# Kernel tuning notes

Hardware: AMD Instinct MI355X
Metric: run time of the kernel (lower is better)

Reference implementation:

```python
import jax, jax.numpy as jnp
import numpy as np
import math

B, N, P, S, C, NC = 8, 20000, 256, 32, 256, 18


def setup_inputs() -> dict:
    key = jax.random.key(0)
    ks = jax.random.split(key, 20)
    w = lambda k, shape: jax.random.normal(k, shape, jnp.float32) * 0.02
    return {
        "xyz": jax.random.normal(ks[0], (B, N, 3), jnp.float32),
        "features": jax.random.normal(ks[1], (B, C, N), jnp.float32),
        "boxes_size": jax.random.uniform(ks[2], (B, P, 3), jnp.float32, 0.2, 1.5),
        "boxes_label": jax.random.normal(ks[3], (B, P, NC), jnp.float32),
        "ts": jax.random.uniform(ks[4], (B,), jnp.float32) * 1000.0,
        "inds": jax.random.randint(ks[5], (B, P), 0, N, jnp.int32),
        # SharedMLP (259 -> 128 -> 128 -> 128), bn=False so conv1x1+bias+ReLU
        "mw0": w(ks[6], (128, C + 3)), "mb0": jnp.zeros((128,), jnp.float32),
        "mw1": w(ks[7], (128, 128)), "mb1": jnp.zeros((128,), jnp.float32),
        "mw2": w(ks[8], (128, 128)), "mb2": jnp.zeros((128,), jnp.float32),
        # label SharedMLP (18+128 -> 256 -> 256 -> 256)
        "lw0": w(ks[9], (256, NC + 128)), "lb0": jnp.zeros((256,), jnp.float32),
        "lw1": w(ks[10], (256, 256)), "lb1": jnp.zeros((256,), jnp.float32),
        "lw2": w(ks[11], (256, 256)), "lb2": jnp.zeros((256,), jnp.float32),
        # time_mlp: sinusoid(128) -> 512 -> GELU -> 512 ; block: SiLU -> 256
        "tw0": w(ks[12], (512, 128)), "tb0": jnp.zeros((512,), jnp.float32),
        "tw1": w(ks[13], (512, 512)), "tb1": jnp.zeros((512,), jnp.float32),
        "bw": w(ks[14], (256, 512)), "bb": jnp.zeros((256,), jnp.float32),
        # time_mlp_label: sinusoid(256) -> 1024 -> GELU -> 1024 ; block: SiLU -> 512
        "tlw0": w(ks[15], (1024, 256)), "tlb0": jnp.zeros((1024,), jnp.float32),
        "tlw1": w(ks[16], (1024, 1024)), "tlb1": jnp.zeros((1024,), jnp.float32),
        "blw": w(ks[17], (512, 1024)), "blb": jnp.zeros((512,), jnp.float32),
    }


def _sinusoid(t, dim):
    half = dim // 2
    freqs = jnp.exp(jnp.arange(half, dtype=jnp.float32) * (-(math.log(10000.0) / (half - 1))))
    e = t[:, None] * freqs[None, :]
    return jnp.concatenate([jnp.sin(e), jnp.cos(e)], axis=-1)


def _film(feat, ts, w0, b0, w1, b1, bw, bb, dim):
    # feat: [B, D, P]; replicates torch repeat_interleave/chunk/reshape exactly
    temb = jax.nn.gelu(_sinusoid(ts, dim) @ w0.T + b0, approximate=False) @ w1.T + b1
    ss = jax.nn.silu(temb) @ bw.T + bb          # [B, 2D]
    ss = jnp.repeat(ss, P, axis=0)              # [B*P, 2D]
    scale, shift = jnp.split(ss, 2, axis=1)
    scale = scale.reshape(-1, P)
    shift = shift.reshape(-1, P)
    f = feat.reshape(-1, P)
    return (f * (scale + 1.0) + shift).reshape(feat.shape[0], -1, P)


def reference(xyz, features, boxes_size, boxes_label, ts, inds,
              mw0, mb0, mw1, mb1, mw2, mb2,
              lw0, lb0, lw1, lb1, lw2, lb2,
              tw0, tb0, tw1, tb1, bw, bb,
              tlw0, tlb0, tlw1, tlb1, blw, blb):
    # gather proposal centers
    new_xyz = jnp.take_along_axis(xyz, inds[:, :, None], axis=1)        # [B,P,3]
    # axis-aligned box containment (the hull corners are an AABB: center +/- size/2)
    half = boxes_size * 0.5
    inside = jnp.all(jnp.abs(xyz[:, None, :, :] - new_xyz[:, :, None, :]) <= half[:, :, None, :], axis=-1)  # [B,P,N]
    # deterministic with-replacement sampling of in-box points: in-box indices first (stable sort), then cycle
    order = jnp.argsort(jnp.logical_not(inside), axis=-1)               # [B,P,N]
    count = jnp.maximum(inside.sum(axis=-1), 1)                          # [B,P]
    pos = jnp.arange(S, dtype=count.dtype)[None, None, :] % count[:, :, None]
    idx = jnp.take_along_axis(order, pos, axis=-1)                       # [B,P,S]
    b_idx = jnp.arange(B)[:, None, None]
    gxyz = xyz[b_idx, idx] - new_xyz[:, :, None, :]                      # [B,P,S,3]
    gfeat = jnp.transpose(features, (0, 2, 1))[b_idx, idx]               # [B,P,S,C]
    g = jnp.concatenate([gxyz, gfeat], axis=-1)                          # [B,P,S,3+C]
    act = lambda x, w, b: jax.nn.relu(jnp.einsum('bpsc,oc->bpso', x, w) + b)
    h = act(act(act(g, mw0, mb0), mw1, mb1), mw2, mb2)                   # [B,P,S,128]
    nf = h.max(axis=2)                                                   # [B,P,128] (max-pool over nsample)
    nf_t = jnp.transpose(nf, (0, 2, 1))                                  # [B,128,P]
    new_features = _film(nf_t, ts, tw0, tb0, tw1, tb1, bw, bb, 128)
    # label branch
    li = jnp.concatenate([boxes_label, nf], axis=-1)                     # [B,P,18+128]
    act2 = lambda x, w, b: jax.nn.relu(jnp.einsum('bpc,oc->bpo', x, w) + b)
    lf = act2(act2(act2(li, lw0, lb0), lw1, lb1), lw2, lb2)              # [B,P,256]
    lf_t = jnp.transpose(lf, (0, 2, 1))                                  # [B,256,P]
    label_feature = _film(lf_t, ts, tlw0, tlb0, tlw1, tlb1, blw, blb, 256)
    return (new_xyz, new_features, label_feature, inds)
```

## Files before the change

kernel.cpp:

```cpp
#include <hip/hip_runtime.h>
#include <math.h>

#define BB 8
#define NN 20000
#define PP 256
#define SSAMP 32
#define CC 256

typedef unsigned short u16;
typedef unsigned int u32;
typedef __attribute__((ext_vector_type(8))) short short8;
typedef __attribute__((ext_vector_type(4))) float f32x4;

__device__ __forceinline__ float b2f(u16 u) {
    union { u32 i; float f; } x; x.i = ((u32)u) << 16; return x.f;
}
__device__ __forceinline__ u16 f2b(float f) {
    union { float f; u32 i; } x; x.f = f;
    u32 i = x.i;
    i += 0x7fffu + ((i >> 16) & 1u);
    return (u16)(i >> 16);
}
__device__ __forceinline__ float rnd_bf(float f) { return b2f(f2b(f)); }
__device__ __forceinline__ float geluf(float x) {
    return 0.5f * x * (1.0f + erff(x * 0.7071067811865476f));
}
__device__ __forceinline__ float siluf(float x) {
    return x / (1.0f + expf(-x));
}
__device__ __forceinline__ f32x4 fz4() { f32x4 z = {0.f,0.f,0.f,0.f}; return z; }

__device__ __forceinline__ float ldf(const void* p, size_t i, int f32f) {
    return f32f ? ((const float*)p)[i] : b2f(((const u16*)p)[i]);
}
__device__ __forceinline__ u16 ldw(const void* p, size_t i, int f32f) {
    return f32f ? f2b(((const float*)p)[i]) : ((const u16*)p)[i];
}

__device__ __forceinline__ int detect_f32d(const void* xyz) {
    int lane = threadIdx.x & 63;
    u16 u = ((const u16*)xyz)[(size_t)lane * 7496];
    int e = (u >> 7) & 0xFF;
    bool inR = (e >= 0x70) && (e <= 0x85);
    unsigned long long m = __ballot(inR);
    return (__popcll(m) < 48) ? 1 : 0;
}

__device__ __forceinline__ void repack_body(int f32f, int rb, int tid,
        const void* mw0, const void* mw1, const void* mw2,
        const void* lw0, const void* lw1, const void* lw2,
        const void* mb0, const void* mb1, const void* mb2,
        const void* lb0, const void* lb1, const void* lb2,
        u16* __restrict__ W0p, u16* __restrict__ W1p, u16* __restrict__ W2p,
        u16* __restrict__ L0p, u16* __restrict__ L1p, u16* __restrict__ L2p,
        float* __restrict__ biasF) {
    int i = rb * 256 + tid;
    if (i < 36864) {
        int o = i / 288, c = i % 288;
        u16 v = 0;
        if (c < 256) v = ldw(mw0, o * 259 + 3 + c, f32f);
        else if (c < 259) v = ldw(mw0, o * 259 + (c - 256), f32f);
        W0p[i] = v;
    } else if (i < 53248) {
        W1p[i - 36864] = ldw(mw1, i - 36864, f32f);
    } else if (i < 69632) {
        W2p[i - 53248] = ldw(mw2, i - 53248, f32f);
    } else if (i < 110592) {
        int j = i - 69632;
        int o = j / 160, c = j % 160;
        L0p[j] = (c < 146) ? ldw(lw0, o * 146 + c, f32f) : (u16)0;
    } else if (i < 176128) {
        L1p[i - 110592] = ldw(lw1, i - 110592, f32f);
    } else if (i < 241664) {
        L2p[i - 176128] = ldw(lw2, i - 176128, f32f);
    } else if (i < 242816) {
        int j = i - 241664;
        float v;
        if (j < 128) v = ldf(mb0, j, f32f);
        else if (j < 256) v = ldf(mb1, j - 128, f32f);
        else if (j < 384) v = ldf(mb2, j - 256, f32f);
        else if (j < 640) v = ldf(lb0, j - 384, f32f);
        else if (j < 896) v = ldf(lb1, j - 640, f32f);
        else v = ldf(lb2, j - 896, f32f);
        biasF[j] = v;
    }
}

__device__ __forceinline__ void transpose_body(int f32f, const void* __restrict__ feat,
        u16* __restrict__ featT, int n0i, int c0i, int bz, int b0, int tid,
        u16 (*tile)[66]) {
    int c0 = c0i * 64, n0 = n0i * 64;
    int b = b0 + bz;
    int tx = tid & 63, ty = tid >> 6;
    const size_t fb = (size_t)b * CC * NN;
    for (int i = 0; i < 16; i++) {
        int cl = ty * 16 + i;
        int n = n0 + tx;
        if (n < NN) tile[cl][tx] = ldw(feat, fb + (size_t)(c0 + cl) * NN + n, f32f);
    }
    __syncthreads();
    const size_t tb = (size_t)bz * NN * CC;
    for (int i = 0; i < 16; i++) {
        int nl = ty * 16 + i;
        int n = n0 + nl;
        if (n < NN) featT[tb + (size_t)n * CC + c0 + tx] = tile[tx][nl];
    }
}

template<int ACT, int SRC>
__device__ __forceinline__ void lin_body(int f32f, const void* __restrict__ xin,
        const void* __restrict__ W, const void* __restrict__ bias,
        float* __restrict__ out, int K, int O, int rb, int tid, float* xs) {
    if (SRC == 2) {
        const float* X = (const float*)xin;
        for (int i = tid; i < 8 * K; i += 256) xs[i] = X[i];
    } else {
        const int half = (SRC == 0) ? 64 : 128;
        const int dim = half * 2;
        const float cst = (SRC == 0) ? (logf(10000.f) / 63.f) : (logf(10000.f) / 127.f);
        for (int i = tid; i < 8 * dim; i += 256) {
            int b = i / dim, j = i % dim;
            float t = ldf(xin, b, f32f);
            int jj = (j < half) ? j : (j - half);
            float e = t * expf(-(float)jj * cst);
            xs[i] = (j < half) ? sinf(e) : cosf(e);
        }
    }
    __syncthreads();
    int lane = tid & 63, wv = tid >> 6;
    int r = rb * 4 + wv;
    if (r >= O) return;
    float acc[8] = {0.f, 0.f, 0.f, 0.f, 0.f, 0.f, 0.f, 0.f};
    for (int k = lane; k < K; k += 64) {
        float wval = ldf(W, (size_t)r * K + k, f32f);
        #pragma unroll
        for (int b = 0; b < 8; b++) acc[b] += wval * xs[b * K + k];
    }
    #pragma unroll
    for (int b = 0; b < 8; b++) {
        acc[b] += __shfl_xor(acc[b], 1);
        acc[b] += __shfl_xor(acc[b], 2);
        acc[b] += __shfl_xor(acc[b], 4);
        acc[b] += __shfl_xor(acc[b], 8);
        acc[b] += __shfl_xor(acc[b], 16);
        acc[b] += __shfl_xor(acc[b], 32);
    }
    if (lane == 0) {
        float bv = ldf(bias, r, f32f);
        #pragma unroll
        for (int b = 0; b < 8; b++) {
            float v = acc[b] + bv;
            if (ACT == 1) v = geluf(v);
            else if (ACT == 2) v = siluf(v);
            out[b * O + r] = v;
        }
    }
}

__device__ __forceinline__ void sample_body(int f32f, const void* __restrict__ xyz,
        const void* __restrict__ bsize, const int* __restrict__ inds,
        int* __restrict__ sidx, float* __restrict__ cenW,
        float* __restrict__ outXyz, float* __restrict__ outInds,
        int pg, int tid, int* sBuf, int* wcnt) {
    int lane = tid & 63, w = tid >> 6;
    int b = pg >> 8;
    int ind = inds[pg];
    ind = ind < 0 ? 0 : (ind >= NN ? NN - 1 : ind);
    if (tid < SSAMP) sBuf[tid] = 0;
    size_t xb = (size_t)b * NN * 3;
    float cx = ldf(xyz, xb + (size_t)ind * 3 + 0, f32f);
    float cy = ldf(xyz, xb + (size_t)ind * 3 + 1, f32f);
    float cz = ldf(xyz, xb + (size_t)ind * 3 + 2, f32f);
    float hx = 0.5f * ldf(bsize, pg * 3 + 0, f32f);
    float hy = 0.5f * ldf(bsize, pg * 3 + 1, f32f);
    float hz = 0.5f * ldf(bsize, pg * 3 + 2, f32f);
    int cnt = 0, par = 0;
    const unsigned long long lmask = (1ull << lane) - 1ull;
    for (int base = 0; base < NN; base += 1024, par ^= 4) {
        int nb = base + w * 256 + lane;
        int nn[4];
        float px[4], py[4], pz[4];
        #pragma unroll
        for (int u = 0; u < 4; u++) {
            int n = nb + u * 64;
            nn[u] = n;
            int nc = n < NN ? n : NN - 1;
            size_t a = xb + (size_t)nc * 3;
            px[u] = ldf(xyz, a, f32f);
            py[u] = ldf(xyz, a + 1, f32f);
            pz[u] = ldf(xyz, a + 2, f32f);
        }
        bool isin[4];
        unsigned long long m[4];
        int pc[4];
        int tw = 0;
        #pragma unroll
        for (int u = 0; u < 4; u++) {
            bool in_ = (nn[u] < NN) &&
                       (fabsf(px[u] - cx) <= hx) &&
                       (fabsf(py[u] - cy) <= hy) &&
                       (fabsf(pz[u] - cz) <= hz);
            isin[u] = in_;
            m[u] = __ballot(in_);
            pc[u] = (int)__popcll(m[u]);
            tw += pc[u];
        }
        if (lane == 0) wcnt[par + w] = tw;
        __syncthreads();
        int w0 = wcnt[par + 0], w1 = wcnt[par + 1], w2 = wcnt[par + 2], w3 = wcnt[par + 3];
        int total = w0 + w1 + w2 + w3;
        int prior = cnt;
        if (w >= 1) prior += w0;
        if (w >= 2) prior += w1;
        if (w >= 3) prior += w2;
        #pragma unroll
        for (int u = 0; u < 4; u++) {
            int pos = prior + (int)__popcll(m[u] & lmask);
            if (isin[u] && pos < SSAMP) sBuf[pos] = nn[u];
            prior += pc[u];
        }
        cnt += total;
        if (cnt >= SSAMP) break;
    }
    __syncthreads();
    int ccap = cnt < SSAMP ? cnt : SSAMP;
    if (ccap < 1) ccap = 1;
    if (tid < SSAMP) sidx[pg * SSAMP + tid] = sBuf[tid % ccap];
    if (tid < 3) {
        float cv = tid == 0 ? cx : (tid == 1 ? cy : cz);
        outXyz[pg * 3 + tid] = cv;
        cenW[pg * 3 + tid] = cv;
    }
    if (tid == 0) outInds[pg] = rnd_bf((float)ind);
}

__global__ __launch_bounds__(256) void k_front(
        const void* __restrict__ xyz, const void* __restrict__ feat,
        const void* __restrict__ bsize, const int* __restrict__ inds,
        const void* __restrict__ ts,
        const void* mw0, const void* mw1, const void* mw2,
        const void* lw0, const void* lw1, const void* lw2,
        const void* mb0, const void* mb1, const void* mb2,
        const void* lb0, const void* lb1, const void* lb2,
        const void* tw0, const void* tb0,
        const void* tlw0, const void* tlb0,
        u16* __restrict__ featT, int nTrans,
        int* __restrict__ sidx, float* __restrict__ cenW,
        float* __restrict__ outXyz, float* __restrict__ outInds,
        u16* __restrict__ W0p, u16* __restrict__ W1p, u16* __restrict__ W2p,
        u16* __restrict__ L0p, u16* __restrict__ L1p, u16* __restrict__ L2p,
        float* __restrict__ biasF, float* __restrict__ h0W, float* __restrict__ g0W) {
    __shared__ __align__(16) char smem[8448];
    int tid = threadIdx.x;
    int f32f = detect_f32d(xyz);
    unsigned bx = blockIdx.x;
    unsigned s1 = 2048u + (unsigned)nTrans;
    unsigned s2 = s1 + 949u;
    unsigned s3 = s2 + 128u;
    if (bx < 2048u) {
        sample_body(f32f, xyz, bsize, inds, sidx, cenW, outXyz, outInds,
                    (int)bx, tid, (int*)smem, (int*)(smem + 128));
    } else if (bx < s1) {
        int t = (int)(bx - 2048u);
        transpose_body(f32f, feat, featT, t % 313, (t / 313) & 3, t / 1252, 0, tid,
                       (u16(*)[66])smem);
    } else if (bx < s2) {
        repack_body(f32f, (int)(bx - s1), tid, mw0, mw1, mw2, lw0, lw1, lw2,
                    mb0, mb1, mb2, lb0, lb1, lb2, W0p, W1p, W2p, L0p, L1p, L2p, biasF);
    } else if (bx < s3) {
        lin_body<1, 0>(f32f, ts, tw0, tb0, h0W, 128, 512, (int)(bx - s2), tid, (float*)smem);
    } else {
        lin_body<1, 1>(f32f, ts, tlw0, tlb0, g0W, 256, 1024, (int)(bx - s3), tid, (float*)smem);
    }
}

__global__ __launch_bounds__(256) void k_mid2(const void* __restrict__ xyz,
        const void* tw1, const void* tb1, const void* tlw1, const void* tlb1,
        const float* __restrict__ h0W, const float* __restrict__ g0W,
        float* __restrict__ tembW, float* __restrict__ temblW) {
    __shared__ float xs[8 * 1024];
    int tid = threadIdx.x;
    int f32f = detect_f32d(xyz);
    unsigned bx = blockIdx.x;
    if (bx < 128u) lin_body<2, 2>(f32f, h0W, tw1, tb1, tembW, 512, 512, (int)bx, tid, xs);
    else lin_body<2, 2>(f32f, g0W, tlw1, tlb1, temblW, 1024, 1024, (int)(bx - 128u), tid, xs);
}

__global__ __launch_bounds__(256) void k_mid3(const void* __restrict__ xyz,
        const void* bw, const void* bb, const void* blw, const void* blb,
        const float* __restrict__ tembW, const float* __restrict__ temblW,
        float* __restrict__ ssW, float* __restrict__ sslW) {
    __shared__ float xs[8 * 1024];
    int tid = threadIdx.x;
    int f32f = detect_f32d(xyz);
    unsigned bx = blockIdx.x;
    if (bx < 64u) lin_body<0, 2>(f32f, tembW, bw, bb, ssW, 512, 256, (int)bx, tid, xs);
    else lin_body<0, 2>(f32f, temblW, blw, blb, sslW, 1024, 512, (int)(bx - 64u), tid, xs);
}

__global__ __launch_bounds__(256) void k_transpose(const void* __restrict__ xyz,
                                                   const void* __restrict__ feat,
                                                   u16* __restrict__ featT, int b0) {
    __shared__ u16 tile[64][66];
    int f32f = detect_f32d(xyz);
    transpose_body(f32f, feat, featT, blockIdx.x, blockIdx.y, blockIdx.z, b0,
                   threadIdx.x, tile);
}

__global__ __launch_bounds__(256) void k_mlp1(
        const u16* __restrict__ featT, const void* __restrict__ feat,
        int blockOff, int tier,
        const void* __restrict__ xyz, const int* __restrict__ sidx,
        const float* __restrict__ cenW, const float* __restrict__ ssW,
        const u16* __restrict__ W0p, const u16* __restrict__ W1p,
        const u16* __restrict__ W2p, const float* __restrict__ biasF,
        u16* __restrict__ nfB, float* __restrict__ outNF) {
    __shared__ u16 gA[64 * 296];
    __shared__ u16 h1s[64 * 136];
    __shared__ int nrowS[64];
    __shared__ float centS[8];
    int f32f = detect_f32d(xyz);
    int tid = threadIdx.x;
    int pbase = (blockIdx.x + blockOff) * 2;
    int b = pbase >> 8;
    if (tid < 64) {
        int n = sidx[pbase * SSAMP + tid];
        nrowS[tid] = n < 0 ? 0 : (n >= NN ? NN - 1 : n);
    }
    if (tid < 6) centS[tid] = cenW[pbase * 3 + tid];
    for (int e = tid; e < 64 * 32; e += 256) {
        int row = e >> 5, c2 = e & 31;
        if (c2 >= 8 && c2 < 28)
            *(u32*)&gA[row * 296 + 256 + (c2 - 8) * 2] = 0u;
    }
    __syncthreads();
    if (tier >= 1) {
        size_t rowBase = (tier == 2) ? ((size_t)b * NN) : 0;
        for (int e = tid; e < 64 * 32; e += 256) {
            int row = e >> 5, seg = e & 31;
            int n = nrowS[row];
            uint4 v = *(const uint4*)(featT + (rowBase + n) * CC + seg * 8);
            *(uint4*)&gA[row * 296 + seg * 8] = v;
        }
    } else {
        int row = tid & 63;
        int n = nrowS[row];
        const size_t fb = (size_t)b * CC * NN;
        int cbase = tid >> 6;
        for (int it = 0; it < 64; it++) {
            int cch = it * 4 + cbase;
            gA[row * 296 + cch] = ldw(feat, fb + (size_t)cch * NN + n, f32f);
        }
    }
    if (tid < 64) {
        int row = tid, q = row >> 5;
        int n = nrowS[row];
        size_t a = ((size_t)b * NN + n) * 3;
        for (int d = 0; d < 3; d++) {
            float gv = ldf(xyz, a + d, f32f) - centS[q * 3 + d];
            gA[row * 296 + 256 + d] = f2b(gv);
        }
    }
    __syncthreads();

    int lane = tid & 63, w = tid >> 6;
    int c15 = lane & 15, kq = lane >> 4;
    f32x4 acc[4][2];

    for (int mt = 0; mt < 4; mt++) for (int j = 0; j < 2; j++) acc[mt][j] = fz4();
    for (int ks = 0; ks < 9; ks++) {
        int k0 = ks * 32 + kq * 8;
        short8 af[4];
        for (int mt = 0; mt < 4; mt++)
            af[mt] = *(const short8*)&gA[(mt * 16 + c15) * 296 + k0];
        for (int j = 0; j < 2; j++) {
            int col = w * 32 + j * 16 + c15;
            short8 bf = *(const short8*)(W0p + col * 288 + k0);
            for (int mt = 0; mt < 4; mt++)
                acc[mt][j] = __builtin_amdgcn_mfma_f32_16x16x32_bf16(af[mt], bf, acc[mt][j], 0, 0, 0);
        }
    }
    for (int j = 0; j < 2; j++) {
        int col = w * 32 + j * 16 + c15;
        float bias = biasF[col];
        for (int mt = 0; mt < 4; mt++)
            for (int r = 0; r < 4; r++) {
                float v = acc[mt][j][r] + bias;
                v = v > 0.f ? v : 0.f;
                h1s[(mt * 16 + kq * 4 + r) * 136 + col] = f2b(v);
            }
    }
    __syncthreads();

    u16* h2s = gA;
    for (int mt = 0; mt < 4; mt++) for (int j = 0; j < 2; j++) acc[mt][j] = fz4();
    for (int ks = 0; ks < 4; ks++) {
        int k0 = ks * 32 + kq * 8;
        short8 af[4];
        for (int mt = 0; mt < 4; mt++)
            af[mt] = *(const short8*)&h1s[(mt * 16 + c15) * 136 + k0];
        for (int j = 0; j < 2; j++) {
            int col = w * 32 + j * 16 + c15;
            short8 bf = *(const short8*)(W1p + col * 128 + k0);
            for (int mt = 0; mt < 4; mt++)
                acc[mt][j] = __builtin_amdgcn_mfma_f32_16x16x32_bf16(af[mt], bf, acc[mt][j], 0, 0, 0);
        }
    }
    __syncthreads();
    for (int j = 0; j < 2; j++) {
        int col = w * 32 + j * 16 + c15;
        float bias = biasF[128 + col];
        for (int mt = 0; mt < 4; mt++)
            for (int r = 0; r < 4; r++) {
                float v = acc[mt][j][r] + bias;
                v = v > 0.f ? v : 0.f;
                h2s[(mt * 16 + kq * 4 + r) * 136 + col] = f2b(v);
            }
    }
    __syncthreads();

    for (int mt = 0; mt < 4; mt++) for (int j = 0; j < 2; j++) acc[mt][j] = fz4();
    for (int ks = 0; ks < 4; ks++) {
        int k0 = ks * 32 + kq * 8;
        short8 af[4];
        for (int mt = 0; mt < 4; mt++)
            af[mt] = *(const short8*)&h2s[(mt * 16 + c15) * 136 + k0];
        for (int j = 0; j < 2; j++) {
            int col = w * 32 + j * 16 + c15;
            short8 bf = *(const short8*)(W2p + col * 128 + k0);
            for (int mt = 0; mt < 4; mt++)
                acc[mt][j] = __builtin_amdgcn_mfma_f32_16x16x32_bf16(af[mt], bf, acc[mt][j], 0, 0, 0);
        }
    }
    int pA = pbase & 255, pB = (pbase + 1) & 255;
    float scA = ssW[b * 256 + (pA & 127)] + 1.f, shA = ssW[b * 256 + 128 + (pA & 127)];
    float scB = ssW[b * 256 + (pB & 127)] + 1.f, shB = ssW[b * 256 + 128 + (pB & 127)];
    for (int j = 0; j < 2; j++) {
        int col = w * 32 + j * 16 + c15;
        float bias = biasF[256 + col];
        float mA = 0.f, mB = 0.f;
        for (int mt = 0; mt < 2; mt++)
            for (int r = 0; r < 4; r++) {
                float v = acc[mt][j][r] + bias; v = v > 0.f ? v : 0.f;
                mA = fmaxf(mA, v);
            }
        for (int mt = 2; mt < 4; mt++)
            for (int r = 0; r < 4; r++) {
                float v = acc[mt][j][r] + bias; v = v > 0.f ? v : 0.f;
                mB = fmaxf(mB, v);
            }
        mA = fmaxf(mA, __shfl_xor(mA, 16)); mA = fmaxf(mA, __shfl_xor(mA, 32));
        mB = fmaxf(mB, __shfl_xor(mB, 16)); mB = fmaxf(mB, __shfl_xor(mB, 32));
        if (lane < 16) {
            nfB[(size_t)(pbase + 0) * 128 + col] = f2b(mA);
            nfB[(size_t)(pbase + 1) * 128 + col] = f2b(mB);
            outNF[((size_t)b * 128 + col) * 256 + pA] = mA * scA + shA;
            outNF[((size_t)b * 128 + col) * 256 + pB] = mB * scB + shB;
        }
    }
}

__global__ __launch_bounds__(256) void k_label(const void* __restrict__ xyz,
        const void* __restrict__ blabel,
        const u16* __restrict__ nfB, const u16* __restrict__ L0p,
        const u16* __restrict__ L1p, const u16* __restrict__ L2p,
        const float* __restrict__ biasF, const float* __restrict__ sslW,
        float* __restrict__ outLF) {
    __shared__ u16 liS[16 * 168];
    __shared__ u16 h1L[16 * 264];
    __shared__ u16 h2L[16 * 264];
    int f32f = detect_f32d(xyz);
    int tid = threadIdx.x;
    int pbase = blockIdx.x * 16;
    for (int e = tid; e < 16 * 160; e += 256) {
        int row = e / 160, c = e % 160;
        int pg = pbase + row;
        u16 v = 0;
        if (c < 18) v = ldw(blabel, pg * 18 + c, f32f);
        else if (c < 146) v = nfB[(size_t)pg * 128 + (c - 18)];
        liS[row * 168 + c] = v;
    }
    __syncthreads();
    int lane = tid & 63, w = tid >> 6;
    int c15 = lane & 15, kq = lane >> 4;
    f32x4 acc[4];

    for (int j = 0; j < 4; j++) acc[j] = fz4();
    for (int ks = 0; ks < 5; ks++) {
        int k0 = ks * 32 + kq * 8;
        short8 af = *(const short8*)&liS[c15 * 168 + k0];
        for (int j = 0; j < 4; j++) {
            int col = w * 64 + j * 16 + c15;
            short8 bf = *(const short8*)(L0p + col * 160 + k0);
            acc[j] = __builtin_amdgcn_mfma_f32_16x16x32_bf16(af, bf, acc[j], 0, 0, 0);
        }
    }
    for (int j = 0; j < 4; j++) {
        int col = w * 64 + j * 16 + c15;
        float bias = biasF[384 + col];
        for (int r = 0; r < 4; r++) {
            float v = acc[j][r] + bias; v = v > 0.f ? v : 0.f;
            h1L[(kq * 4 + r) * 264 + col] = f2b(v);
        }
    }
    __syncthreads();

    for (int j = 0; j < 4; j++) acc[j] = fz4();
    for (int ks = 0; ks < 8; ks++) {
        int k0 = ks * 32 + kq * 8;
        short8 af = *(const short8*)&h1L[c15 * 264 + k0];
        for (int j = 0; j < 4; j++) {
            int col = w * 64 + j * 16 + c15;
            short8 bf = *(const short8*)(L1p + col * 256 + k0);
            acc[j] = __builtin_amdgcn_mfma_f32_16x16x32_bf16(af, bf, acc[j], 0, 0, 0);
        }
    }
    for (int j = 0; j < 4; j++) {
        int col = w * 64 + j * 16 + c15;
        float bias = biasF[640 + col];
        for (int r = 0; r < 4; r++) {
            float v = acc[j][r] + bias; v = v > 0.f ? v : 0.f;
            h2L[(kq * 4 + r) * 264 + col] = f2b(v);
        }
    }
    __syncthreads();

    for (int j = 0; j < 4; j++) acc[j] = fz4();
    for (int ks = 0; ks < 8; ks++) {
        int k0 = ks * 32 + kq * 8;
        short8 af = *(const short8*)&h2L[c15 * 264 + k0];
        for (int j = 0; j < 4; j++) {
            int col = w * 64 + j * 16 + c15;
            short8 bf = *(const short8*)(L2p + col * 256 + k0);
            acc[j] = __builtin_amdgcn_mfma_f32_16x16x32_bf16(af, bf, acc[j], 0, 0, 0);
        }
    }
    for (int j = 0; j < 4; j++) {
        int col = w * 64 + j * 16 + c15;
        float bias = biasF[896 + col];
        for (int r = 0; r < 4; r++) {
            int pr = pbase + kq * 4 + r;
            int bb2 = pr >> 8, p = pr & 255;
            float v = acc[j][r] + bias; v = v > 0.f ? v : 0.f;
            float sc = sslW[bb2 * 512 + p] + 1.f;
            float sh = sslW[bb2 * 512 + 256 + p];
            outLF[((size_t)bb2 * 256 + col) * 256 + p] = v * sc + sh;
        }
    }
}

extern "C" void kernel_launch(void* const* d_in, const int* in_sizes, int n_in,
                              void* d_out, int out_size, void* d_ws, size_t ws_size,
                              hipStream_t stream) {
    const void* xyz    = d_in[0];
    const void* feat   = d_in[1];
    const void* bsize  = d_in[2];
    const void* blabel = d_in[3];
    const void* ts     = d_in[4];
    const int* inds    = (const int*)d_in[5];
    const void* mw0 = d_in[6];  const void* mb0 = d_in[7];
    const void* mw1 = d_in[8];  const void* mb1 = d_in[9];
    const void* mw2 = d_in[10]; const void* mb2 = d_in[11];
    const void* lw0 = d_in[12]; const void* lb0 = d_in[13];
    const void* lw1 = d_in[14]; const void* lb1 = d_in[15];
    const void* lw2 = d_in[16]; const void* lb2 = d_in[17];
    const void* tw0 = d_in[18]; const void* tb0 = d_in[19];
    const void* tw1 = d_in[20]; const void* tb1 = d_in[21];
    const void* bw  = d_in[22]; const void* bb  = d_in[23];
    const void* tlw0 = d_in[24]; const void* tlb0 = d_in[25];
    const void* tlw1 = d_in[26]; const void* tlb1 = d_in[27];
    const void* blw  = d_in[28]; const void* blb  = d_in[29];

    float* out = (float*)d_out;
    float* outXyz  = out;
    float* outNF   = out + 6144;
    float* outLF   = out + 268288;
    float* outInds = out + 792576;

    char* ws = (char*)d_ws;
    u16*   W0p   = (u16*)(ws + 64);
    u16*   W1p   = (u16*)(ws + 73792);
    u16*   W2p   = (u16*)(ws + 106560);
    u16*   L0p   = (u16*)(ws + 139328);
    u16*   L1p   = (u16*)(ws + 221248);
    u16*   L2p   = (u16*)(ws + 352320);
    float* biasF = (float*)(ws + 483392);
    float* ssW   = (float*)(ws + 488000);
    float* sslW  = (float*)(ws + 496192);
    float* cenW  = (float*)(ws + 512576);
    int*   sidx  = (int*)(ws + 537152);
    u16*   nfB   = (u16*)(ws + 799296);
    float* h0W   = (float*)(ws + 1323584);
    float* tembW = (float*)(ws + 1339968);
    float* g0W   = (float*)(ws + 1356352);
    float* temblW= (float*)(ws + 1389120);
    u16*   featT = (u16*)(ws + 1421888);
    const size_t NEED_A = 1421888ull + 81920000ull;
    const size_t NEED_B = 1421888ull + 10240000ull;
    int tier = (ws_size >= NEED_A) ? 2 : ((ws_size >= NEED_B) ? 1 : 0);

    int nTrans = (tier == 2) ? 10016 : 0;
    unsigned gFront = 2048u + (unsigned)nTrans + 949u + 128u + 256u;
    k_front<<<dim3(gFront), dim3(256), 0, stream>>>(
        xyz, feat, bsize, inds, ts,
        mw0, mw1, mw2, lw0, lw1, lw2,
        mb0, mb1, mb2, lb0, lb1, lb2,
        tw0, tb0, tlw0, tlb0,
        featT, nTrans, sidx, cenW, outXyz, outInds,
        W0p, W1p, W2p, L0p, L1p, L2p, biasF, h0W, g0W);

    k_mid2<<<dim3(384), dim3(256), 0, stream>>>(xyz, tw1, tb1, tlw1, tlb1,
                                                h0W, g0W, tembW, temblW);
    k_mid3<<<dim3(192), dim3(256), 0, stream>>>(xyz, bw, bb, blw, blb,
                                                tembW, temblW, ssW, sslW);

    if (tier == 2) {
        k_mlp1<<<dim3(1024), dim3(256), 0, stream>>>(featT, feat, 0, 2, xyz, sidx, cenW, ssW,
                                                     W0p, W1p, W2p, biasF, nfB, outNF);
    } else if (tier == 1) {
        for (int b = 0; b < BB; b++) {
            k_transpose<<<dim3(313, 4, 1), dim3(256), 0, stream>>>(xyz, feat, featT, b);
            k_mlp1<<<dim3(128), dim3(256), 0, stream>>>(featT, feat, b * 128, 1, xyz, sidx, cenW, ssW,
                                                        W0p, W1p, W2p, biasF, nfB, outNF);
        }
    } else {
        k_mlp1<<<dim3(1024), dim3(256), 0, stream>>>(featT, feat, 0, 0, xyz, sidx, cenW, ssW,
                                                     W0p, W1p, W2p, biasF, nfB, outNF);
    }

    k_label<<<dim3(128), dim3(256), 0, stream>>>(xyz, blabel, nfB, L0p, L1p, L2p, biasF, sslW, outLF);
}
```

Measured before the change: 427.5 us.

## Vectorize transpose, prefetch sampling loads, and merge MLP with time-MLP kernels

Several changes at once. The feature transpose now uses float4/ushort4 vector loads and stores for full tiles. The ball-query loop double-buffers the next xyz chunk in registers. The grouped point MLP is fused into one kernel with the second time-MLP layer, and the FiLM scale/shift of new_features is deferred to the tail kernel through an fp32 staging buffer. This cuts launches and lets the point MLP overlap the time-embedding GEMV. The cost is an extra global round-trip for the unmodulated features, plus higher register and LDS use in the merged kernel.

```diff
diff --git a/kernel.cpp b/kernel.cpp
--- a/kernel.cpp
+++ b/kernel.cpp
@@ -91,19 +91,58 @@
         u16 (*tile)[66]) {
     int c0 = c0i * 64, n0 = n0i * 64;
     int b = b0 + bz;
-    int tx = tid & 63, ty = tid >> 6;
     const size_t fb = (size_t)b * CC * NN;
-    for (int i = 0; i < 16; i++) {
-        int cl = ty * 16 + i;
-        int n = n0 + tx;
-        if (n < NN) tile[cl][tx] = ldw(feat, fb + (size_t)(c0 + cl) * NN + n, f32f);
-    }
-    __syncthreads();
     const size_t tb = (size_t)bz * NN * CC;
-    for (int i = 0; i < 16; i++) {
-        int nl = ty * 16 + i;
-        int n = n0 + nl;
-        if (n < NN) featT[tb + (size_t)n * CC + c0 + tx] = tile[tx][nl];
+    if (n0 + 64 <= NN) {
+        int n4 = tid & 15, ci = tid >> 4;
+        if (f32f) {
+            #pragma unroll
+            for (int pass = 0; pass < 4; pass++) {
+                int c = pass * 16 + ci;
+                const float* src = (const float*)feat + fb + (size_t)(c0 + c) * NN + n0 + n4 * 4;
+                float4 v = *(const float4*)src;
+                tile[c][n4 * 4 + 0] = f2b(v.x);
+                tile[c][n4 * 4 + 1] = f2b(v.y);
+                tile[c][n4 * 4 + 2] = f2b(v.z);
+                tile[c][n4 * 4 + 3] = f2b(v.w);
+            }
+        } else {
+            #pragma unroll
+            for (int pass = 0; pass < 4; pass++) {
+                int c = pass * 16 + ci;
+                const u16* src = (const u16*)feat + fb + (size_t)(c0 + c) * NN + n0 + n4 * 4;
+                ushort4 v = *(const ushort4*)src;
+                tile[c][n4 * 4 + 0] = v.x;
+                tile[c][n4 * 4 + 1] = v.y;
+                tile[c][n4 * 4 + 2] = v.z;
+                tile[c][n4 * 4 + 3] = v.w;
+            }
+        }
+        __syncthreads();
+        int c4 = tid & 15, ni = tid >> 4;
+        #pragma unroll
+        for (int pass = 0; pass < 4; pass++) {
+            int n = pass * 16 + ni;
+            ushort4 o;
+            o.x = tile[c4 * 4 + 0][n];
+            o.y = tile[c4 * 4 + 1][n];
+            o.z = tile[c4 * 4 + 2][n];
+            o.w = tile[c4 * 4 + 3][n];
+            *(ushort4*)(featT + tb + (size_t)(n0 + n) * CC + c0 + c4 * 4) = o;
+        }
+    } else {
+        int tx = tid & 63, ty = tid >> 6;
+        for (int i = 0; i < 16; i++) {
+            int cl = ty * 16 + i;
+            int n = n0 + tx;
+            if (n < NN) tile[cl][tx] = ldw(feat, fb + (size_t)(c0 + cl) * NN + n, f32f);
+        }
+        __syncthreads();
+        for (int i = 0; i < 16; i++) {
+            int nl = ty * 16 + i;
+            int n = n0 + nl;
+            if (n < NN) featT[tb + (size_t)n * CC + c0 + tx] = tile[tx][nl];
+        }
     }
 }
 
@@ -176,19 +215,34 @@
     float hz = 0.5f * ldf(bsize, pg * 3 + 2, f32f);
     int cnt = 0, par = 0;
     const unsigned long long lmask = (1ull << lane) - 1ull;
-    for (int base = 0; base < NN; base += 1024, par ^= 4) {
-        int nb = base + w * 256 + lane;
-        int nn[4];
-        float px[4], py[4], pz[4];
-        #pragma unroll
-        for (int u = 0; u < 4; u++) {
-            int n = nb + u * 64;
-            nn[u] = n;
-            int nc = n < NN ? n : NN - 1;
-            size_t a = xb + (size_t)nc * 3;
-            px[u] = ldf(xyz, a, f32f);
-            py[u] = ldf(xyz, a + 1, f32f);
-            pz[u] = ldf(xyz, a + 2, f32f);
+    int nn[4];
+    float px[4], py[4], pz[4];
+    #pragma unroll
+    for (int u = 0; u < 4; u++) {
+        int n = w * 256 + lane + u * 64;
+        nn[u] = n;
+        int nc = n < NN ? n : NN - 1;
+        size_t a = xb + (size_t)nc * 3;
+        px[u] = ldf(xyz, a, f32f);
+        py[u] = ldf(xyz, a + 1, f32f);
+        pz[u] = ldf(xyz, a + 2, f32f);
+    }
+    for (int base = 0;;) {
+        int nbase = base + 1024;
+        bool more = nbase < NN;
+        int qn[4];
+        float qx[4], qy[4], qz[4];
+        if (more) {
+            #pragma unroll
+            for (int u = 0; u < 4; u++) {
+                int n = nbase + w * 256 + lane + u * 64;
+                qn[u] = n;
+                int nc = n < NN ? n : NN - 1;
+                size_t a = xb + (size_t)nc * 3;
+                qx[u] = ldf(xyz, a, f32f);
+                qy[u] = ldf(xyz, a + 1, f32f);
+                qz[u] = ldf(xyz, a + 2, f32f);
+            }
         }
         bool isin[4];
         unsigned long long m[4];
@@ -220,7 +274,13 @@
             prior += pc[u];
         }
         cnt += total;
-        if (cnt >= SSAMP) break;
+        if (cnt >= SSAMP || !more) break;
+        par ^= 4;
+        base = nbase;
+        #pragma unroll
+        for (int u = 0; u < 4; u++) {
+            nn[u] = qn[u]; px[u] = qx[u]; py[u] = qy[u]; pz[u] = qz[u];
+        }
     }
     __syncthreads();
     int ccap = cnt < SSAMP ? cnt : SSAMP;
@@ -232,6 +292,153 @@
         cenW[pg * 3 + tid] = cv;
     }
     if (tid == 0) outInds[pg] = rnd_bf((float)ind);
+}
+
+__device__ __forceinline__ void mlp1_body(int f32f,
+        const u16* __restrict__ featT, const void* __restrict__ feat,
+        int pbase, int tier,
+        const void* __restrict__ xyz, const int* __restrict__ sidx,
+        const float* __restrict__ cenW,
+        const u16* __restrict__ W0p, const u16* __restrict__ W1p,
+        const u16* __restrict__ W2p, const float* __restrict__ biasF,
+        u16* __restrict__ nfB, float* __restrict__ nfF,
+        int tid, u16* gA, int* nrowS, float* centS) {
+    int b = pbase >> 8;
+    if (tid < 64) {
+        int n = sidx[pbase * SSAMP + tid];
+        nrowS[tid] = n < 0 ? 0 : (n >= NN ? NN - 1 : n);
+    }
+    if (tid < 6) centS[tid] = cenW[pbase * 3 + tid];
+    for (int e = tid; e < 64 * 32; e += 256) {
+        int row = e >> 5, c2 = e & 31;
+        if (c2 >= 8 && c2 < 28)
+            *(u32*)&gA[row * 296 + 256 + (c2 - 8) * 2] = 0u;
+    }
+    __syncthreads();
+    if (tier >= 1) {
+        size_t rowBase = (tier == 2) ? ((size_t)b * NN) : 0;
+        for (int e = tid; e < 64 * 32; e += 256) {
+            int row = e >> 5, seg = e & 31;
+            int n = nrowS[row];
+            uint4 v = *(const uint4*)(featT + (rowBase + n) * CC + seg * 8);
+            *(uint4*)&gA[row * 296 + seg * 8] = v;
+        }
+    } else {
+        int row = tid & 63;
+        int n = nrowS[row];
+        const size_t fb = (size_t)b * CC * NN;
+        int cbase = tid >> 6;
+        for (int it = 0; it < 64; it++) {
+            int cch = it * 4 + cbase;
+            gA[row * 296 + cch] = ldw(feat, fb + (size_t)cch * NN + n, f32f);
+        }
+    }
+    if (tid < 64) {
+        int row = tid, q = row >> 5;
+        int n = nrowS[row];
+        size_t a = ((size_t)b * NN + n) * 3;
+        for (int d = 0; d < 3; d++) {
+            float gv = ldf(xyz, a + d, f32f) - centS[q * 3 + d];
+            gA[row * 296 + 256 + d] = f2b(gv);
+        }
+    }
+    __syncthreads();
+
+    int lane = tid & 63, w = tid >> 6;
+    int c15 = lane & 15, kq = lane >> 4;
+    f32x4 acc[4][2];
+
+    for (int mt = 0; mt < 4; mt++) for (int j = 0; j < 2; j++) acc[mt][j] = fz4();
+    for (int ks = 0; ks < 9; ks++) {
+        int k0 = ks * 32 + kq * 8;
+        short8 af[4];
+        for (int mt = 0; mt < 4; mt++)
+            af[mt] = *(const short8*)&gA[(mt * 16 + c15) * 296 + k0];
+        for (int j = 0; j < 2; j++) {
+            int col = w * 32 + j * 16 + c15;
+            short8 bf = *(const short8*)(W0p + col * 288 + k0);
+            for (int mt = 0; mt < 4; mt++)
+                acc[mt][j] = __builtin_amdgcn_mfma_f32_16x16x32_bf16(af[mt], bf, acc[mt][j], 0, 0, 0);
+        }
+    }
+    __syncthreads();
+    u16* h1s = gA;
+    u16* h2s = gA + 8704;
+    for (int j = 0; j < 2; j++) {
+        int col = w * 32 + j * 16 + c15;
+        float bias = biasF[col];
+        for (int mt = 0; mt < 4; mt++)
+            for (int r = 0; r < 4; r++) {
+                float v = acc[mt][j][r] + bias;
+                v = v > 0.f ? v : 0.f;
+                h1s[(mt * 16 + kq * 4 + r) * 136 + col] = f2b(v);
+            }
+    }
+    __syncthreads();
+
+    for (int mt = 0; mt < 4; mt++) for (int j = 0; j < 2; j++) acc[mt][j] = fz4();
+    for (int ks = 0; ks < 4; ks++) {
+        int k0 = ks * 32 + kq * 8;
+        short8 af[4];
+        for (int mt = 0; mt < 4; mt++)
+            af[mt] = *(const short8*)&h1s[(mt * 16 + c15) * 136 + k0];
+        for (int j = 0; j < 2; j++) {
+            int col = w * 32 + j * 16 + c15;
+            short8 bf = *(const short8*)(W1p + col * 128 + k0);
+            for (int mt = 0; mt < 4; mt++)
+                acc[mt][j] = __builtin_amdgcn_mfma_f32_16x16x32_bf16(af[mt], bf, acc[mt][j], 0, 0, 0);
+        }
+    }
+    __syncthreads();
+    for (int j = 0; j < 2; j++) {
+        int col = w * 32 + j * 16 + c15;
+        float bias = biasF[128 + col];
+        for (int mt = 0; mt < 4; mt++)
+            for (int r = 0; r < 4; r++) {
+                float v = acc[mt][j][r] + bias;
+                v = v > 0.f ? v : 0.f;
+                h2s[(mt * 16 + kq * 4 + r) * 136 + col] = f2b(v);
+            }
+    }
+    __syncthreads();
+
+    for (int mt = 0; mt < 4; mt++) for (int j = 0; j < 2; j++) acc[mt][j] = fz4();
+    for (int ks = 0; ks < 4; ks++) {
+        int k0 = ks * 32 + kq * 8;
+        short8 af[4];
+        for (int mt = 0; mt < 4; mt++)
+            af[mt] = *(const short8*)&h2s[(mt * 16 + c15) * 136 + k0];
+        for (int j = 0; j < 2; j++) {
+            int col = w * 32 + j * 16 + c15;
+            short8 bf = *(const short8*)(W2p + col * 128 + k0);
+            for (int mt = 0; mt < 4; mt++)
+                acc[mt][j] = __builtin_amdgcn_mfma_f32_16x16x32_bf16(af[mt], bf, acc[mt][j], 0, 0, 0);
+        }
+    }
+    int pA = pbase & 255, pB = (pbase + 1) & 255;
+    for (int j = 0; j < 2; j++) {
+        int col = w * 32 + j * 16 + c15;
+        float bias = biasF[256 + col];
+        float mA = 0.f, mB = 0.f;
+        for (int mt = 0; mt < 2; mt++)
+            for (int r = 0; r < 4; r++) {
+                float v = acc[mt][j][r] + bias; v = v > 0.f ? v : 0.f;
+                mA = fmaxf(mA, v);
+            }
+        for (int mt = 2; mt < 4; mt++)
+            for (int r = 0; r < 4; r++) {
+                float v = acc[mt][j][r] + bias; v = v > 0.f ? v : 0.f;
+                mB = fmaxf(mB, v);
+            }
+        mA = fmaxf(mA, __shfl_xor(mA, 16)); mA = fmaxf(mA, __shfl_xor(mA, 32));
+        mB = fmaxf(mB, __shfl_xor(mB, 16)); mB = fmaxf(mB, __shfl_xor(mB, 32));
+        if (lane < 16) {
+            nfB[(size_t)(pbase + 0) * 128 + col] = f2b(mA);
+            nfB[(size_t)(pbase + 1) * 128 + col] = f2b(mB);
+            nfF[((size_t)b * 128 + col) * 256 + pA] = mA;
+            nfF[((size_t)b * 128 + col) * 256 + pB] = mB;
+        }
+    }
 }
 
 __global__ __launch_bounds__(256) void k_front(
@@ -254,16 +461,16 @@
     int tid = threadIdx.x;
     int f32f = detect_f32d(xyz);
     unsigned bx = blockIdx.x;
-    unsigned s1 = 2048u + (unsigned)nTrans;
+    unsigned s1 = (unsigned)nTrans + 2048u;
     unsigned s2 = s1 + 949u;
     unsigned s3 = s2 + 128u;
-    if (bx < 2048u) {
-        sample_body(f32f, xyz, bsize, inds, sidx, cenW, outXyz, outInds,
-                    (int)bx, tid, (int*)smem, (int*)(smem + 128));
-    } else if (bx < s1) {
-        int t = (int)(bx - 2048u);
+    if (bx < (unsigned)nTrans) {
+        int t = (int)bx;
         transpose_body(f32f, feat, featT, t % 313, (t / 313) & 3, t / 1252, 0, tid,
                        (u16(*)[66])smem);
+    } else if (bx < s1) {
+        sample_body(f32f, xyz, bsize, inds, sidx, cenW, outXyz, outInds,
+                    (int)(bx - (unsigned)nTrans), tid, (int*)smem, (int*)(smem + 128));
     } else if (bx < s2) {
         repack_body(f32f, (int)(bx - s1), tid, mw0, mw1, mw2, lw0, lw1, lw2,
                     mb0, mb1, mb2, lb0, lb1, lb2, W0p, W1p, W2p, L0p, L1p, L2p, biasF);
@@ -274,19 +481,33 @@
     }
 }
 
-__global__ __launch_bounds__(256) void k_mid2(const void* __restrict__ xyz,
+__global__ __launch_bounds__(256) void k_mid(int nMlp, int blockOff, int tier,
+        const u16* __restrict__ featT, const void* __restrict__ feat,
+        const void* __restrict__ xyz, const int* __restrict__ sidx,
+        const float* __restrict__ cenW,
+        const u16* __restrict__ W0p, const u16* __restrict__ W1p,
+        const u16* __restrict__ W2p, const float* __restrict__ biasF,
+        u16* __restrict__ nfB, float* __restrict__ nfF,
         const void* tw1, const void* tb1, const void* tlw1, const void* tlb1,
         const float* __restrict__ h0W, const float* __restrict__ g0W,
         float* __restrict__ tembW, float* __restrict__ temblW) {
-    __shared__ float xs[8 * 1024];
+    __shared__ __align__(16) char smem[38176];
     int tid = threadIdx.x;
     int f32f = detect_f32d(xyz);
-    unsigned bx = blockIdx.x;
-    if (bx < 128u) lin_body<2, 2>(f32f, h0W, tw1, tb1, tembW, 512, 512, (int)bx, tid, xs);
-    else lin_body<2, 2>(f32f, g0W, tlw1, tlb1, temblW, 1024, 1024, (int)(bx - 128u), tid, xs);
-}
-
-__global__ __launch_bounds__(256) void k_mid3(const void* __restrict__ xyz,
+    int bx = (int)blockIdx.x;
+    if (bx < nMlp) {
+        mlp1_body(f32f, featT, feat, (bx + blockOff) * 2, tier, xyz, sidx, cenW,
+                  W0p, W1p, W2p, biasF, nfB, nfF, tid,
+                  (u16*)smem, (int*)(smem + 37888), (float*)(smem + 38144));
+    } else {
+        int lb = bx - nMlp;
+        float* xs = (float*)smem;
+        if (lb < 128) lin_body<2, 2>(f32f, h0W, tw1, tb1, tembW, 512, 512, lb, tid, xs);
+        else lin_body<2, 2>(f32f, g0W, tlw1, tlb1, temblW, 1024, 1024, lb - 128, tid, xs);
+    }
+}
+
+__global__ __launch_bounds__(256) void k_lin3(const void* __restrict__ xyz,
         const void* bw, const void* bb, const void* blw, const void* blb,
         const float* __restrict__ tembW, const float* __restrict__ temblW,
         float* __restrict__ ssW, float* __restrict__ sslW) {
@@ -307,171 +528,34 @@
                    threadIdx.x, tile);
 }
 
-__global__ __launch_bounds__(256) void k_mlp1(
-        const u16* __restrict__ featT, const void* __restrict__ feat,
-        int blockOff, int tier,
-        const void* __restrict__ xyz, const int* __restrict__ sidx,
-        const float* __restrict__ cenW, const float* __restrict__ ssW,
-        const u16* __restrict__ W0p, const u16* __restrict__ W1p,
-        const u16* __restrict__ W2p, const float* __restrict__ biasF,
-        u16* __restrict__ nfB, float* __restrict__ outNF) {
-    __shared__ u16 gA[64 * 296];
-    __shared__ u16 h1s[64 * 136];
-    __shared__ int nrowS[64];
-    __shared__ float centS[8];
-    int f32f = detect_f32d(xyz);
-    int tid = threadIdx.x;
-    int pbase = (blockIdx.x + blockOff) * 2;
-    int b = pbase >> 8;
-    if (tid < 64) {
-        int n = sidx[pbase * SSAMP + tid];
-        nrowS[tid] = n < 0 ? 0 : (n >= NN ? NN - 1 : n);
-    }
-    if (tid < 6) centS[tid] = cenW[pbase * 3 + tid];
-    for (int e = tid; e < 64 * 32; e += 256) {
-        int row = e >> 5, c2 = e & 31;
-        if (c2 >= 8 && c2 < 28)
-            *(u32*)&gA[row * 296 + 256 + (c2 - 8) * 2] = 0u;
-    }
-    __syncthreads();
-    if (tier >= 1) {
-        size_t rowBase = (tier == 2) ? ((size_t)b * NN) : 0;
-        for (int e = tid; e < 64 * 32; e += 256) {
-            int row = e >> 5, seg = e & 31;
-            int n = nrowS[row];
-            uint4 v = *(const uint4*)(featT + (rowBase + n) * CC + seg * 8);
-            *(uint4*)&gA[row * 296 + seg * 8] = v;
-        }
-    } else {
-        int row = tid & 63;
-        int n = nrowS[row];
-        const size_t fb = (size_t)b * CC * NN;
-        int cbase = tid >> 6;
-        for (int it = 0; it < 64; it++) {
-            int cch = it * 4 + cbase;
-            gA[row * 296 + cch] = ldw(feat, fb + (size_t)cch * NN + n, f32f);
-        }
-    }
-    if (tid < 64) {
-        int row = tid, q = row >> 5;
-        int n = nrowS[row];
-        size_t a = ((size_t)b * NN + n) * 3;
-        for (int d = 0; d < 3; d++) {
-            float gv = ldf(xyz, a + d, f32f) - centS[q * 3 + d];
-            gA[row * 296 + 256 + d] = f2b(gv);
-        }
-    }
-    __syncthreads();
-
-    int lane = tid & 63, w = tid >> 6;
-    int c15 = lane & 15, kq = lane >> 4;
-    f32x4 acc[4][2];
-
-    for (int mt = 0; mt < 4; mt++) for (int j = 0; j < 2; j++) acc[mt][j] = fz4();
-    for (int ks = 0; ks < 9; ks++) {
-        int k0 = ks * 32 + kq * 8;
-        short8 af[4];
-        for (int mt = 0; mt < 4; mt++)
-            af[mt] = *(const short8*)&gA[(mt * 16 + c15) * 296 + k0];
-        for (int j = 0; j < 2; j++) {
-            int col = w * 32 + j * 16 + c15;
-            short8 bf = *(const short8*)(W0p + col * 288 + k0);
-            for (int mt = 0; mt < 4; mt++)
-                acc[mt][j] = __builtin_amdgcn_mfma_f32_16x16x32_bf16(af[mt], bf, acc[mt][j], 0, 0, 0);
-        }
-    }
-    for (int j = 0; j < 2; j++) {
-        int col = w * 32 + j * 16 + c15;
-        float bias = biasF[col];
-        for (int mt = 0; mt < 4; mt++)
-            for (int r = 0; r < 4; r++) {
-                float v = acc[mt][j][r] + bias;
-                v = v > 0.f ? v : 0.f;
-                h1s[(mt * 16 + kq * 4 + r) * 136 + col] = f2b(v);
-            }
-    }
-    __syncthreads();
-
-    u16* h2s = gA;
-    for (int mt = 0; mt < 4; mt++) for (int j = 0; j < 2; j++) acc[mt][j] = fz4();
-    for (int ks = 0; ks < 4; ks++) {
-        int k0 = ks * 32 + kq * 8;
-        short8 af[4];
-        for (int mt = 0; mt < 4; mt++)
-            af[mt] = *(const short8*)&h1s[(mt * 16 + c15) * 136 + k0];
-        for (int j = 0; j < 2; j++) {
-            int col = w * 32 + j * 16 + c15;
-            short8 bf = *(const short8*)(W1p + col * 128 + k0);
-            for (int mt = 0; mt < 4; mt++)
-                acc[mt][j] = __builtin_amdgcn_mfma_f32_16x16x32_bf16(af[mt], bf, acc[mt][j], 0, 0, 0);
-        }
-    }
-    __syncthreads();
-    for (int j = 0; j < 2; j++) {
-        int col = w * 32 + j * 16 + c15;
-        float bias = biasF[128 + col];
-        for (int mt = 0; mt < 4; mt++)
-            for (int r = 0; r < 4; r++) {
-                float v = acc[mt][j][r] + bias;
-                v = v > 0.f ? v : 0.f;
-                h2s[(mt * 16 + kq * 4 + r) * 136 + col] = f2b(v);
-            }
-    }
-    __syncthreads();
-
-    for (int mt = 0; mt < 4; mt++) for (int j = 0; j < 2; j++) acc[mt][j] = fz4();
-    for (int ks = 0; ks < 4; ks++) {
-        int k0 = ks * 32 + kq * 8;
-        short8 af[4];
-        for (int mt = 0; mt < 4; mt++)
-            af[mt] = *(const short8*)&h2s[(mt * 16 + c15) * 136 + k0];
-        for (int j = 0; j < 2; j++) {
-            int col = w * 32 + j * 16 + c15;
-            short8 bf = *(const short8*)(W2p + col * 128 + k0);
-            for (int mt = 0; mt < 4; mt++)
-                acc[mt][j] = __builtin_amdgcn_mfma_f32_16x16x32_bf16(af[mt], bf, acc[mt][j], 0, 0, 0);
-        }
-    }
-    int pA = pbase & 255, pB = (pbase + 1) & 255;
-    float scA = ssW[b * 256 + (pA & 127)] + 1.f, shA = ssW[b * 256 + 128 + (pA & 127)];
-    float scB = ssW[b * 256 + (pB & 127)] + 1.f, shB = ssW[b * 256 + 128 + (pB & 127)];
-    for (int j = 0; j < 2; j++) {
-        int col = w * 32 + j * 16 + c15;
-        float bias = biasF[256 + col];
-        float mA = 0.f, mB = 0.f;
-        for (int mt = 0; mt < 2; mt++)
-            for (int r = 0; r < 4; r++) {
-                float v = acc[mt][j][r] + bias; v = v > 0.f ? v : 0.f;
-                mA = fmaxf(mA, v);
-            }
-        for (int mt = 2; mt < 4; mt++)
-            for (int r = 0; r < 4; r++) {
-                float v = acc[mt][j][r] + bias; v = v > 0.f ? v : 0.f;
-                mB = fmaxf(mB, v);
-            }
-        mA = fmaxf(mA, __shfl_xor(mA, 16)); mA = fmaxf(mA, __shfl_xor(mA, 32));
-        mB = fmaxf(mB, __shfl_xor(mB, 16)); mB = fmaxf(mB, __shfl_xor(mB, 32));
-        if (lane < 16) {
-            nfB[(size_t)(pbase + 0) * 128 + col] = f2b(mA);
-            nfB[(size_t)(pbase + 1) * 128 + col] = f2b(mB);
-            outNF[((size_t)b * 128 + col) * 256 + pA] = mA * scA + shA;
-            outNF[((size_t)b * 128 + col) * 256 + pB] = mB * scB + shB;
-        }
-    }
-}
-
-__global__ __launch_bounds__(256) void k_label(const void* __restrict__ xyz,
+__global__ __launch_bounds__(256) void k_tail(const void* __restrict__ xyz,
         const void* __restrict__ blabel,
         const u16* __restrict__ nfB, const u16* __restrict__ L0p,
         const u16* __restrict__ L1p, const u16* __restrict__ L2p,
         const float* __restrict__ biasF, const float* __restrict__ sslW,
-        float* __restrict__ outLF) {
+        const float* __restrict__ ssW, const float* __restrict__ nfF,
+        float* __restrict__ outLF, float* __restrict__ outNF) {
     __shared__ u16 liS[16 * 168];
     __shared__ u16 h1L[16 * 264];
     __shared__ u16 h2L[16 * 264];
     int f32f = detect_f32d(xyz);
     int tid = threadIdx.x;
-    int pbase = blockIdx.x * 16;
+    unsigned bxu = blockIdx.x;
+    if (bxu >= 128u) {
+        int base = (int)(bxu - 128u) * 4096;
+        #pragma unroll
+        for (int i = 0; i < 16; i++) {
+            int idx = base + i * 256 + tid;
+            int p = idx & 255;
+            int cb = idx >> 8;
+            int b = cb >> 7;
+            float sc = ssW[b * 256 + (p & 127)] + 1.f;
+            float sh = ssW[b * 256 + 128 + (p & 127)];
+            outNF[idx] = nfF[idx] * sc + sh;
+        }
+        return;
+    }
+    int pbase = (int)bxu * 16;
     for (int e = tid; e < 16 * 160; e += 256) {
         int row = e / 160, c = e % 160;
         int pg = pbase + row;
@@ -594,13 +678,14 @@
     float* tembW = (float*)(ws + 1339968);
     float* g0W   = (float*)(ws + 1356352);
     float* temblW= (float*)(ws + 1389120);
-    u16*   featT = (u16*)(ws + 1421888);
-    const size_t NEED_A = 1421888ull + 81920000ull;
-    const size_t NEED_B = 1421888ull + 10240000ull;
+    float* nfF   = (float*)(ws + 1421888);
+    u16*   featT = (u16*)(ws + 2470464);
+    const size_t NEED_A = 2470464ull + 81920000ull;
+    const size_t NEED_B = 2470464ull + 10240000ull;
     int tier = (ws_size >= NEED_A) ? 2 : ((ws_size >= NEED_B) ? 1 : 0);
 
     int nTrans = (tier == 2) ? 10016 : 0;
-    unsigned gFront = 2048u + (unsigned)nTrans + 949u + 128u + 256u;
+    unsigned gFront = (unsigned)nTrans + 2048u + 949u + 128u + 256u;
     k_front<<<dim3(gFront), dim3(256), 0, stream>>>(
         xyz, feat, bsize, inds, ts,
         mw0, mw1, mw2, lw0, lw1, lw2,
@@ -609,24 +694,29 @@
         featT, nTrans, sidx, cenW, outXyz, outInds,
         W0p, W1p, W2p, L0p, L1p, L2p, biasF, h0W, g0W);
 
-    k_mid2<<<dim3(384), dim3(256), 0, stream>>>(xyz, tw1, tb1, tlw1, tlb1,
-                                                h0W, g0W, tembW, temblW);
-    k_mid3<<<dim3(192), dim3(256), 0, stream>>>(xyz, bw, bb, blw, blb,
-                                                tembW, temblW, ssW, sslW);
-
     if (tier == 2) {
-        k_mlp1<<<dim3(1024), dim3(256), 0, stream>>>(featT, feat, 0, 2, xyz, sidx, cenW, ssW,
-                                                     W0p, W1p, W2p, biasF, nfB, outNF);
+        k_mid<<<dim3(1024 + 384), dim3(256), 0, stream>>>(1024, 0, 2,
+            featT, feat, xyz, sidx, cenW, W0p, W1p, W2p, biasF, nfB, nfF,
+            tw1, tb1, tlw1, tlb1, h0W, g0W, tembW, temblW);
     } else if (tier == 1) {
         for (int b = 0; b < BB; b++) {
             k_transpose<<<dim3(313, 4, 1), dim3(256), 0, stream>>>(xyz, feat, featT, b);
-            k_mlp1<<<dim3(128), dim3(256), 0, stream>>>(featT, feat, b * 128, 1, xyz, sidx, cenW, ssW,
-                                                        W0p, W1p, W2p, biasF, nfB, outNF);
-        }
+            k_mid<<<dim3(128), dim3(256), 0, stream>>>(128, b * 128, 1,
+                featT, feat, xyz, sidx, cenW, W0p, W1p, W2p, biasF, nfB, nfF,
+                tw1, tb1, tlw1, tlb1, h0W, g0W, tembW, temblW);
+        }
+        k_mid<<<dim3(384), dim3(256), 0, stream>>>(0, 0, 1,
+            featT, feat, xyz, sidx, cenW, W0p, W1p, W2p, biasF, nfB, nfF,
+            tw1, tb1, tlw1, tlb1, h0W, g0W, tembW, temblW);
     } else {
-        k_mlp1<<<dim3(1024), dim3(256), 0, stream>>>(featT, feat, 0, 0, xyz, sidx, cenW, ssW,
-                                                     W0p, W1p, W2p, biasF, nfB, outNF);
-    }
-
-    k_label<<<dim3(128), dim3(256), 0, stream>>>(xyz, blabel, nfB, L0p, L1p, L2p, biasF, sslW, outLF);
-}
+        k_mid<<<dim3(1024 + 384), dim3(256), 0, stream>>>(1024, 0, 0,
+            featT, feat, xyz, sidx, cenW, W0p, W1p, W2p, biasF, nfB, nfF,
+            tw1, tb1, tlw1, tlb1, h0W, g0W, tembW, temblW);
+    }
+
+    k_lin3<<<dim3(192), dim3(256), 0, stream>>>(xyz, bw, bb, blw, blb,
+                                                tembW, temblW, ssW, sslW);
+
+    k_tail<<<dim3(128 + 64), dim3(256), 0, stream>>>(xyz, blabel, nfB,
+        L0p, L1p, L2p, biasF, sslW, ssW, nfF, outLF, outNF);
+}
```

New measurement: 423.8 us. No clear change (-0.9%).
